# Kernel tuning notes

Measured on AMD Instinct MI355X. Metric: run time of the kernel, lower is better.

The kernel has to match this reference:

```python
import jax, jax.numpy as jnp
import numpy as np

N = 50000        # nodes
E = 800000       # edges (before self-loops)
IN = 128         # in_channels
HID = 32         # hidden_channels
HEADS = 8        # num_heads
G = 64           # num graphs in batch
NEG_SLOPE = 0.2  # PyG GATConv default


def setup_inputs() -> dict:
    key = jax.random.key(0)
    ks = jax.random.split(key, 12)
    x = jax.random.normal(ks[0], (N, IN), jnp.float32)
    edge_index = jax.random.randint(ks[1], (2, E), 0, N, jnp.int32)
    edge_attr = jax.random.normal(ks[2], (E, 4), jnp.float32)
    batch = jnp.sort(jax.random.randint(ks[3], (N,), 0, G, jnp.int32))
    s = 0.05
    # GATConv 1: in -> HEADS*HID
    W1 = jax.random.normal(ks[4], (IN, HEADS * HID), jnp.float32) * s
    a_src1 = jax.random.normal(ks[5], (HEADS, HID), jnp.float32) * s
    a_dst1 = jax.random.normal(ks[6], (HEADS, HID), jnp.float32) * s
    b1 = jnp.zeros((HEADS * HID,), jnp.float32)
    # GATConv 2: HEADS*HID -> HID (heads=1)
    W2 = jax.random.normal(ks[7], (HEADS * HID, HID), jnp.float32) * s
    a_src2 = jax.random.normal(ks[8], (1, HID), jnp.float32) * s
    a_dst2 = jax.random.normal(ks[9], (1, HID), jnp.float32) * s
    b2 = jnp.zeros((HID,), jnp.float32)
    return {"x": x, "edge_index": edge_index, "edge_attr": edge_attr, "batch": batch,
            "W1": W1, "a_src1": a_src1, "a_dst1": a_dst1, "b1": b1,
            "W2": W2, "a_src2": a_src2, "a_dst2": a_dst2, "b2": b2}


def gat_conv(x, src, dst, W, a_src, a_dst, b):
    # x: [N, F_in]; W: [F_in, H*C]; a_src/a_dst: [H, C]
    H, C = a_src.shape
    h = (x @ W).reshape(N, H, C)                      # [N, H, C]
    al_s = jnp.einsum('nhc,hc->nh', h, a_src)         # [N, H]
    al_d = jnp.einsum('nhc,hc->nh', h, a_dst)
    e = jax.nn.leaky_relu(al_s[src] + al_d[dst], NEG_SLOPE)  # [Etot, H]
    # segment softmax over incoming edges of each dst node
    m = jax.ops.segment_max(e, dst, num_segments=N)
    p = jnp.exp(e - m[dst])
    z = jax.ops.segment_sum(p, dst, num_segments=N)
    alpha = p / z[dst]                                # [Etot, H]
    out = jax.ops.segment_sum(alpha[:, :, None] * h[src], dst, num_segments=N)
    return out.reshape(N, H * C) + b


def reference(x, edge_index, edge_attr, batch, W1, a_src1, a_dst1, b1, W2, a_src2, a_dst2, b2):
    # edge_attr is ignored: GATConv was built without edge_dim (PyG lin_edge=None).
    loops = jnp.arange(N, dtype=edge_index.dtype)     # PyG add_self_loops=True
    src = jnp.concatenate([edge_index[0], loops])
    dst = jnp.concatenate([edge_index[1], loops])
    h = jax.nn.relu(gat_conv(x, src, dst, W1, a_src1, a_dst1, b1))
    # dropout p=0.2 is identity in eval mode
    h = gat_conv(h, src, dst, W2, a_src2, a_dst2, b2)  # [N, HID]
    # global_mean_pool over graph ids
    sums = jax.ops.segment_sum(h, batch, num_segments=G)
    cnts = jax.ops.segment_sum(jnp.ones((N, 1), h.dtype), batch, num_segments=G)
    return sums / jnp.maximum(cnts, 1.0)              # [G, HID]
```

## Files before the change

### kernel.cpp

```cpp
#include <hip/hip_runtime.h>
#include <hip/hip_bf16.h>

#define NNODES 50000
#define NEDGES 800000
#define FIN 128
#define HID 32
#define HEADS 8
#define NG 64
#define NEG_SLOPE 0.2f
#define MAXDEG 64

using bf16x8 = __attribute__((ext_vector_type(8))) short;
using f32x4  = __attribute__((ext_vector_type(4))) float;
using f32x2  = __attribute__((ext_vector_type(2))) float;

static __device__ __forceinline__ float leaky(float x) {
    return x > 0.f ? x : NEG_SLOPE * x;
}
static __device__ __forceinline__ unsigned short f2bf(float f) {
    unsigned int x = __float_as_uint(f);
    return (unsigned short)((x + 0x7FFFu + ((x >> 16) & 1u)) >> 16);
}
static __device__ __forceinline__ unsigned int pack2bf(float lo, float hi) {
    return (unsigned int)f2bf(lo) | ((unsigned int)f2bf(hi) << 16);
}
static __device__ __forceinline__ float bfl(unsigned int u) {
    return __uint_as_float(u << 16);
}
static __device__ __forceinline__ float bfh(unsigned int u) {
    return __uint_as_float(u & 0xFFFF0000u);
}
static __device__ __forceinline__ float bfs(unsigned short u) {
    return __uint_as_float((unsigned int)u << 16);
}
static __device__ __forceinline__ unsigned char f2fp8(float f) {
    return (unsigned char)(__builtin_amdgcn_cvt_pk_fp8_f32(f, f, 0, false) & 0xFF);
}

#define ZERO_BLOCKS 196
__global__ void zero_swz_kernel(int* __restrict__ cnt,
                                const float* __restrict__ W1, const float* __restrict__ W2,
                                const float* __restrict__ a_src1, const float* __restrict__ a_dst1,
                                unsigned short* __restrict__ w1s,
                                unsigned short* __restrict__ w2s,
                                unsigned short* __restrict__ w1al) {
    if (blockIdx.x < ZERO_BLOCKS) {
        int i = blockIdx.x * 256 + threadIdx.x;
        if (i < NNODES) cnt[i] = 0;
        return;
    }
    int idx = (blockIdx.x - ZERO_BLOCKS) * 256 + threadIdx.x;
    if (idx < 32768) {
        int j    = idx & 7;
        int lane = (idx >> 3) & 63;
        int ks   = (idx >> 9) & 3;
        int ct   = idx >> 11;
        int k = ks * 32 + (lane >> 4) * 8 + j;
        int n = ct * 16 + (lane & 15);
        w1s[idx] = f2bf(W1[k * 256 + n]);
    } else if (idx < 32768 + 8192) {
        int id2  = idx - 32768;
        int j    = id2 & 7;
        int lane = (id2 >> 3) & 63;
        int ks   = (id2 >> 9) & 7;
        int ct   = id2 >> 12;
        int k = ks * 32 + (lane >> 4) * 8 + j;
        int n = ct * 16 + (lane & 15);
        w2s[id2] = f2bf(W2[k * 32 + n]);
    } else if (idx < 32768 + 8192 + 2048) {
        int id3  = idx - 40960;
        int j    = id3 & 7;
        int lane = (id3 >> 3) & 63;
        int ks   = id3 >> 9;
        int k = ks * 32 + (lane >> 4) * 8 + j;
        int c = lane & 15;
        int h = c & 7;
        const float* av = (c < 8) ? a_src1 : a_dst1;
        float v = 0.f;
#pragma unroll 8
        for (int cc = 0; cc < 32; ++cc)
            v += W1[k * 256 + h * 32 + cc] * av[h * 32 + cc];
        w1al[id3] = f2bf(v);
    }
}

#define SCAT_GROUPS 782
__global__ void scatter_kernel(const int* __restrict__ ei, int* __restrict__ cnt,
                               unsigned short* __restrict__ csr) {
    int xcd = blockIdx.x & 7;
    int slice = blockIdx.x >> 3;
    int e4 = slice * 256 + threadIdx.x;
    int dlo = xcd * 6250;
    int dhi = dlo + 6250;
    if (e4 < NEDGES / 4) {
        int4 d = *(const int4*)(ei + NEDGES + e4 * 4);
        int4 s;
        bool a0 = d.x >= dlo && d.x < dhi;
        bool a1 = d.y >= dlo && d.y < dhi;
        bool a2 = d.z >= dlo && d.z < dhi;
        bool a3 = d.w >= dlo && d.w < dhi;
        if (a0 | a1 | a2 | a3) s = *(const int4*)(ei + e4 * 4);
        if (a0) { int p = atomicAdd(&cnt[d.x], 1); csr[(d.x << 6) + p] = (unsigned short)s.x; }
        if (a1) { int p = atomicAdd(&cnt[d.y], 1); csr[(d.y << 6) + p] = (unsigned short)s.y; }
        if (a2) { int p = atomicAdd(&cnt[d.z], 1); csr[(d.z << 6) + p] = (unsigned short)s.z; }
        if (a3) { int p = atomicAdd(&cnt[d.w], 1); csr[(d.w << 6) + p] = (unsigned short)s.w; }
    }
}

__global__ __launch_bounds__(256) void gemm1_mfma_kernel(const float* __restrict__ x,
                                                         const unsigned short* __restrict__ w1s,
                                                         const unsigned short* __restrict__ w1al,
                                                         unsigned char* __restrict__ h1f8,
                                                         float* __restrict__ al_s,
                                                         float* __restrict__ al_d) {
    int t = threadIdx.x;
    int w = t >> 6;
    int l = t & 63;
    int lane16 = l & 15, quad = l >> 4;

    bf16x8 bf[4][4];
    const bf16x8* wp = (const bf16x8*)w1s;
#pragma unroll
    for (int ct = 0; ct < 4; ++ct)
#pragma unroll
        for (int ks = 0; ks < 4; ++ks)
            bf[ct][ks] = wp[((w * 4 + ct) * 4 + ks) * 64 + l];

    bf16x8 bf_al[4];
    if (w == 0) {
        const bf16x8* ap = (const bf16x8*)w1al;
#pragma unroll
        for (int ks = 0; ks < 4; ++ks)
            bf_al[ks] = ap[ks * 64 + l];
    }

    int rbase = blockIdx.x * 64;
    for (int rg = 0; rg < 4; ++rg) {
        int row0 = rbase + rg * 16;
        int r = row0 + lane16;
        int r_eff = r < NNODES ? r : NNODES - 1;
        bf16x8 af[4];
#pragma unroll
        for (int ks = 0; ks < 4; ++ks) {
            const float* ap = x + (size_t)r_eff * FIN + ks * 32 + quad * 8;
            float4 a0 = *(const float4*)ap;
            float4 a1 = *(const float4*)(ap + 4);
            bf16x8 v;
            v[0] = (short)f2bf(a0.x); v[1] = (short)f2bf(a0.y);
            v[2] = (short)f2bf(a0.z); v[3] = (short)f2bf(a0.w);
            v[4] = (short)f2bf(a1.x); v[5] = (short)f2bf(a1.y);
            v[6] = (short)f2bf(a1.z); v[7] = (short)f2bf(a1.w);
            af[ks] = v;
        }
        f32x4 acc[4];
#pragma unroll
        for (int ct = 0; ct < 4; ++ct) acc[ct] = (f32x4){0.f, 0.f, 0.f, 0.f};
#pragma unroll
        for (int ks = 0; ks < 4; ++ks)
#pragma unroll
            for (int ct = 0; ct < 4; ++ct)
                acc[ct] = __builtin_amdgcn_mfma_f32_16x16x32_bf16(af[ks], bf[ct][ks], acc[ct], 0, 0, 0);

        if (w == 0) {
            f32x4 aal = (f32x4){0.f, 0.f, 0.f, 0.f};
#pragma unroll
            for (int ks = 0; ks < 4; ++ks)
                aal = __builtin_amdgcn_mfma_f32_16x16x32_bf16(af[ks], bf_al[ks], aal, 0, 0, 0);
#pragma unroll
            for (int reg = 0; reg < 4; ++reg) {
                int gr = row0 + quad * 4 + reg;
                if (gr < NNODES) {
                    if (lane16 < 8) al_s[gr * HEADS + lane16] = aal[reg];
                    else            al_d[gr * HEADS + lane16 - 8] = aal[reg];
                }
            }
        }

#pragma unroll
        for (int ct = 0; ct < 4; ++ct)
#pragma unroll
            for (int reg = 0; reg < 4; ++reg) {
                int gr = row0 + quad * 4 + reg;
                if (gr < NNODES)
                    h1f8[(size_t)gr * 256 + w * 64 + ct * 16 + lane16] = f2fp8(acc[ct][reg]);
            }
    }
}

__global__ __launch_bounds__(256) void gather1_kernel(const unsigned char* __restrict__ h1f8,
                                                      const float* __restrict__ al_s,
                                                      const float* __restrict__ al_d,
                                                      const int* __restrict__ cnt,
                                                      const unsigned short* __restrict__ csr,
                                                      const float* __restrict__ b1,
                                                      unsigned short* __restrict__ out1b) {
    int t = threadIdx.x;
    int l = t & 63;
    int q = l & 31;
    int base = l & 32;
    int n = blockIdx.x * 8 + (t >> 5);
    int e_st = q >> 3;
    int h_st = q & 7;
    int h_f  = q >> 2;
    float ad_st = al_d[n * HEADS + h_st];

    float p = __expf(leaky(al_s[n * HEADS + h_f] + al_d[n * HEADS + h_f]));
    float z = p;
    f32x2 acc01, acc23, acc45, acc67;
    {
        uint2 v = *(const uint2*)(h1f8 + (size_t)n * 256 + q * 8);
        f32x2 pp = (f32x2){p, p};
        acc01 = pp * __builtin_amdgcn_cvt_pk_f32_fp8(v.x, false);
        acc23 = pp * __builtin_amdgcn_cvt_pk_f32_fp8(v.x, true);
        acc45 = pp * __builtin_amdgcn_cvt_pk_f32_fp8(v.y, false);
        acc67 = pp * __builtin_amdgcn_cvt_pk_f32_fp8(v.y, true);
    }

    int beg = n << 6;
    int end = beg + cnt[n];
    for (int i = beg; i < end; i += 4) {
        int rem = end - i;
        int src4 = n;
        float pe4 = 0.f;
        if (e_st < rem) {
            src4 = csr[i + e_st];
            pe4 = __expf(leaky(al_s[src4 * HEADS + h_st] + ad_st));
        }
#pragma unroll
        for (int j = 0; j < 4; ++j) {
            int   sj  = __shfl(src4, base + j * 8);
            float pej = __shfl(pe4, base + j * 8 + h_f);
            uint2 v = *(const uint2*)(h1f8 + (size_t)sj * 256 + q * 8);
            z += pej;
            f32x2 pj = (f32x2){pej, pej};
            acc01 += pj * __builtin_amdgcn_cvt_pk_f32_fp8(v.x, false);
            acc23 += pj * __builtin_amdgcn_cvt_pk_f32_fp8(v.x, true);
            acc45 += pj * __builtin_amdgcn_cvt_pk_f32_fp8(v.y, false);
            acc67 += pj * __builtin_amdgcn_cvt_pk_f32_fp8(v.y, true);
        }
    }
    float inv = 1.0f / z;
    float4 b0 = *(const float4*)(b1 + q * 8);
    float4 b2 = *(const float4*)(b1 + q * 8 + 4);
    float o[8];
    o[0] = acc01[0] * inv + b0.x; o[1] = acc01[1] * inv + b0.y;
    o[2] = acc23[0] * inv + b0.z; o[3] = acc23[1] * inv + b0.w;
    o[4] = acc45[0] * inv + b2.x; o[5] = acc45[1] * inv + b2.y;
    o[6] = acc67[0] * inv + b2.z; o[7] = acc67[1] * inv + b2.w;
#pragma unroll
    for (int k = 0; k < 8; ++k) o[k] = o[k] > 0.f ? o[k] : 0.f;
    uint4 pk;
    pk.x = pack2bf(o[0], o[1]); pk.y = pack2bf(o[2], o[3]);
    pk.z = pack2bf(o[4], o[5]); pk.w = pack2bf(o[6], o[7]);
    *(uint4*)(out1b + (size_t)n * 256 + q * 8) = pk;
}

__global__ __launch_bounds__(256) void gemm2_mfma_kernel(const unsigned short* __restrict__ out1b,
                                                         const unsigned short* __restrict__ w2s,
                                                         const float* __restrict__ a_src,
                                                         const float* __restrict__ a_dst,
                                                         unsigned short* __restrict__ h2b,
                                                         float* __restrict__ al_s,
                                                         float* __restrict__ al_d) {
    int t = threadIdx.x;
    int w = t >> 6;
    int l = t & 63;
    int lane16 = l & 15, quad = l >> 4;

    bf16x8 bf[2][8];
    const bf16x8* wp = (const bf16x8*)w2s;
#pragma unroll
    for (int ct = 0; ct < 2; ++ct)
#pragma unroll
        for (int ks = 0; ks < 8; ++ks)
            bf[ct][ks] = wp[((ct * 8 + ks)) * 64 + l];

    float as_c[2], ad_c[2];
#pragma unroll
    for (int ct = 0; ct < 2; ++ct) {
        as_c[ct] = a_src[ct * 16 + lane16];
        ad_c[ct] = a_dst[ct * 16 + lane16];
    }

    int row0 = blockIdx.x * 64 + w * 16;
    int r = row0 + lane16;
    int r_eff = r < NNODES ? r : NNODES - 1;
    f32x4 acc[2];
    acc[0] = (f32x4){0.f, 0.f, 0.f, 0.f};
    acc[1] = (f32x4){0.f, 0.f, 0.f, 0.f};
#pragma unroll
    for (int ks = 0; ks < 8; ++ks) {
        bf16x8 af = *(const bf16x8*)(out1b + (size_t)r_eff * 256 + ks * 32 + quad * 8);
        acc[0] = __builtin_amdgcn_mfma_f32_16x16x32_bf16(af, bf[0][ks], acc[0], 0, 0, 0);
        acc[1] = __builtin_amdgcn_mfma_f32_16x16x32_bf16(af, bf[1][ks], acc[1], 0, 0, 0);
    }
#pragma unroll
    for (int reg = 0; reg < 4; ++reg) {
        int gr = row0 + quad * 4 + reg;
        if (gr < NNODES) {
            h2b[(size_t)gr * 32 + lane16]      = f2bf(acc[0][reg]);
            h2b[(size_t)gr * 32 + 16 + lane16] = f2bf(acc[1][reg]);
        }
        float ps = acc[0][reg] * as_c[0] + acc[1][reg] * as_c[1];
        float pd = acc[0][reg] * ad_c[0] + acc[1][reg] * ad_c[1];
#pragma unroll
        for (int m = 1; m < 16; m <<= 1) {
            ps += __shfl_xor(ps, m);
            pd += __shfl_xor(pd, m);
        }
        if (lane16 == 0 && gr < NNODES) {
            al_s[gr] = ps;
            al_d[gr] = pd;
        }
    }
}

__global__ __launch_bounds__(256) void gather2_kernel(const unsigned short* __restrict__ h2b,
                                                      const float* __restrict__ al_s,
                                                      const float* __restrict__ al_d,
                                                      const int* __restrict__ cnt,
                                                      const unsigned short* __restrict__ csr,
                                                      const float* __restrict__ b2,
                                                      float* __restrict__ out2) {
    int t = threadIdx.x;
    int l = t & 63;
    int e_sl = l & 15;
    int base = l & 48;
    int c0 = (l & 15) * 2;
    int n = blockIdx.x * 16 + (t >> 4);

    float ad = al_d[n];
    float p = __expf(leaky(al_s[n] + ad));
    float z = p;
    float acc0, acc1;
    {
        unsigned int v = *(const unsigned int*)(h2b + (size_t)n * HID + c0);
        acc0 = p * bfl(v);
        acc1 = p * bfh(v);
    }
    int beg = n << 6;
    int end = beg + cnt[n];
    for (int i = beg; i < end; i += 16) {
        int rem = end - i;
        int src = n;
        float pe = 0.f;
        if (e_sl < rem) {
            src = csr[i + e_sl];
            pe = __expf(leaky(al_s[src] + ad));
        }
        int m = rem < 16 ? rem : 16;
        for (int j0 = 0; j0 < m; j0 += 8) {
#pragma unroll
            for (int jj = 0; jj < 8; ++jj) {
                int   sj  = __shfl(src, base + j0 + jj);
                float pej = __shfl(pe, base + j0 + jj);
                unsigned int v = *(const unsigned int*)(h2b + (size_t)sj * HID + c0);
                z += pej;
                acc0 += pej * bfl(v);
                acc1 += pej * bfh(v);
            }
        }
    }
    float inv = 1.0f / z;
    float2 o;
    o.x = acc0 * inv + b2[c0];
    o.y = acc1 * inv + b2[c0 + 1];
    *(float2*)(out2 + (size_t)n * HID + c0) = o;
}

__global__ __launch_bounds__(256) void pool_kernel(const float* __restrict__ out2,
                                                   const int* __restrict__ batch,
                                                   float* __restrict__ out) {
    __shared__ float red[256];
    int g = blockIdx.x;
    int t = threadIdx.x;
    int c = t & 31;
    int sub = t >> 5;
    int beg, end;
    {
        int lo = 0, hi = NNODES;
        while (lo < hi) { int mid = (lo + hi) >> 1; if (batch[mid] < g) lo = mid + 1; else hi = mid; }
        beg = lo;
        lo = beg; hi = NNODES;
        while (lo < hi) { int mid = (lo + hi) >> 1; if (batch[mid] < g + 1) lo = mid + 1; else hi = mid; }
        end = lo;
    }
    float s = 0.f;
    for (int n = beg + sub; n < end; n += 8) s += out2[n * HID + c];
    red[t] = s;
    __syncthreads();
    if (t < 32) {
        float tot = 0.f;
#pragma unroll
        for (int k = 0; k < 8; ++k) tot += red[c + 32 * k];
        int cnt2 = end - beg;
        out[g * HID + c] = tot / (float)(cnt2 > 0 ? cnt2 : 1);
    }
}

extern "C" void kernel_launch(void* const* d_in, const int* in_sizes, int n_in,
                              void* d_out, int out_size, void* d_ws, size_t ws_size,
                              hipStream_t stream) {
    const float* x      = (const float*)d_in[0];
    const int*   ei     = (const int*)d_in[1];
    const int*   batch  = (const int*)d_in[3];
    const float* W1     = (const float*)d_in[4];
    const float* a_src1 = (const float*)d_in[5];
    const float* a_dst1 = (const float*)d_in[6];
    const float* b1     = (const float*)d_in[7];
    const float* W2     = (const float*)d_in[8];
    const float* a_src2 = (const float*)d_in[9];
    const float* a_dst2 = (const float*)d_in[10];
    const float* b2     = (const float*)d_in[11];
    float* out = (float*)d_out;

    char* ws = (char*)d_ws;
    size_t off = 0;
    auto alloc = [&](size_t bytes) {
        size_t o = off;
        off = (off + bytes + 255) & ~(size_t)255;
        return o;
    };
    unsigned char*  h1f8  = (unsigned char*)(ws + alloc((size_t)NNODES * 256));
    unsigned short* out1b = (unsigned short*)(ws + alloc((size_t)NNODES * 256 * 2));
    unsigned short* h2b   = (unsigned short*)(ws + alloc((size_t)NNODES * HID * 2));
    unsigned short* w1s   = (unsigned short*)(ws + alloc((size_t)16 * 4 * 64 * 8 * 2));
    unsigned short* w2s   = (unsigned short*)(ws + alloc((size_t)2 * 8 * 64 * 8 * 2));
    unsigned short* w1al  = (unsigned short*)(ws + alloc((size_t)4 * 64 * 8 * 2));
    float* out2   = (float*)(ws + alloc((size_t)NNODES * HID * 4));
    float* al_s1  = (float*)(ws + alloc((size_t)NNODES * HEADS * 4));
    float* al_d1  = (float*)(ws + alloc((size_t)NNODES * HEADS * 4));
    float* al_s2  = (float*)(ws + alloc((size_t)NNODES * 4));
    float* al_d2  = (float*)(ws + alloc((size_t)NNODES * 4));
    int*   cnt    = (int*)(ws + alloc((size_t)NNODES * 4));
    unsigned short* csr = (unsigned short*)(ws + alloc((size_t)NNODES * MAXDEG * 2));
    (void)ws_size;

    zero_swz_kernel<<<ZERO_BLOCKS + 168, 256, 0, stream>>>(cnt, W1, W2, a_src1, a_dst1,
                                                           w1s, w2s, w1al);
    scatter_kernel<<<SCAT_GROUPS * 8, 256, 0, stream>>>(ei, cnt, csr);

    gemm1_mfma_kernel<<<(NNODES + 63) / 64, 256, 0, stream>>>(x, w1s, w1al,
                                                              h1f8, al_s1, al_d1);
    gather1_kernel<<<NNODES / 8, 256, 0, stream>>>(h1f8, al_s1, al_d1, cnt, csr, b1, out1b);

    gemm2_mfma_kernel<<<(NNODES + 63) / 64, 256, 0, stream>>>(out1b, w2s, a_src2, a_dst2,
                                                              h2b, al_s2, al_d2);
    gather2_kernel<<<NNODES / 16, 256, 0, stream>>>(h2b, al_s2, al_d2, cnt, csr, b2, out2);
    pool_kernel<<<NG, 256, 0, stream>>>(out2, batch, out);
}
```

Before: 253.6 us.

## Partition layer-1 features by head pair and pin partitions to XCDs

Layer-1 fp8 features are stored head-pair-major (four 64-byte planes per node), and the attention logits are stored head-major. Each gather block handles one head pair for 32 nodes, and the block index is mapped so that every XCD reads only one 3.2 MB feature plane, which should keep that plane resident in its L2. The change also uses nontemporal loads for CSR indices and nontemporal stores for the output. In exchange, each node's CSR list and exp computations are now repeated across four head-pair blocks, and each edge gather reads a 64-byte segment instead of a full 256-byte row.

```diff
diff --git a/kernel.cpp b/kernel.cpp
--- a/kernel.cpp
+++ b/kernel.cpp
@@ -13,6 +13,7 @@
 using bf16x8 = __attribute__((ext_vector_type(8))) short;
 using f32x4  = __attribute__((ext_vector_type(4))) float;
 using f32x2  = __attribute__((ext_vector_type(2))) float;
+using u32x4  = __attribute__((ext_vector_type(4))) unsigned int;
 
 static __device__ __forceinline__ float leaky(float x) {
     return x > 0.f ? x : NEG_SLOPE * x;
@@ -110,7 +111,7 @@
 __global__ __launch_bounds__(256) void gemm1_mfma_kernel(const float* __restrict__ x,
                                                          const unsigned short* __restrict__ w1s,
                                                          const unsigned short* __restrict__ w1al,
-                                                         unsigned char* __restrict__ h1f8,
+                                                         unsigned char* __restrict__ h1p,
                                                          float* __restrict__ al_s,
                                                          float* __restrict__ al_d) {
     int t = threadIdx.x;
@@ -170,8 +171,8 @@
             for (int reg = 0; reg < 4; ++reg) {
                 int gr = row0 + quad * 4 + reg;
                 if (gr < NNODES) {
-                    if (lane16 < 8) al_s[gr * HEADS + lane16] = aal[reg];
-                    else            al_d[gr * HEADS + lane16 - 8] = aal[reg];
+                    if (lane16 < 8) al_s[(size_t)lane16 * NNODES + gr] = aal[reg];
+                    else            al_d[(size_t)(lane16 - 8) * NNODES + gr] = aal[reg];
                 }
             }
         }
@@ -182,33 +183,41 @@
             for (int reg = 0; reg < 4; ++reg) {
                 int gr = row0 + quad * 4 + reg;
                 if (gr < NNODES)
-                    h1f8[(size_t)gr * 256 + w * 64 + ct * 16 + lane16] = f2fp8(acc[ct][reg]);
+                    h1p[((size_t)w * NNODES + gr) * 64 + ct * 16 + lane16] = f2fp8(acc[ct][reg]);
             }
     }
 }
 
-__global__ __launch_bounds__(256) void gather1_kernel(const unsigned char* __restrict__ h1f8,
+__global__ __launch_bounds__(256) void gather1_kernel(const unsigned char* __restrict__ h1p,
                                                       const float* __restrict__ al_s,
                                                       const float* __restrict__ al_d,
                                                       const int* __restrict__ cnt,
                                                       const unsigned short* __restrict__ csr,
                                                       const float* __restrict__ b1,
                                                       unsigned short* __restrict__ out1b) {
+    int b = blockIdx.x;
+    int xcd = b & 7;
+    int hp = xcd >> 1;
+    int g = (b >> 3) * 2 + (xcd & 1);
     int t = threadIdx.x;
     int l = t & 63;
-    int q = l & 31;
-    int base = l & 32;
-    int n = blockIdx.x * 8 + (t >> 5);
-    int e_st = q >> 3;
-    int h_st = q & 7;
-    int h_f  = q >> 2;
-    float ad_st = al_d[n * HEADS + h_st];
-
-    float p = __expf(leaky(al_s[n * HEADS + h_f] + al_d[n * HEADS + h_f]));
+    int base = l & 56;
+    int rr = l & 7;
+    int hs = rr >> 2;
+    int e_slot = rr & 3;
+    int n = g * 32 + (t >> 3);
+    if (n >= NNODES) return;
+
+    int h = hp * 2 + hs;
+    const float* als_h = al_s + (size_t)h * NNODES;
+    float ad = al_d[(size_t)h * NNODES + n];
+    const unsigned char* hrow = h1p + (size_t)hp * NNODES * 64;
+
+    float p = __expf(leaky(als_h[n] + ad));
     float z = p;
     f32x2 acc01, acc23, acc45, acc67;
     {
-        uint2 v = *(const uint2*)(h1f8 + (size_t)n * 256 + q * 8);
+        uint2 v = *(const uint2*)(hrow + (size_t)n * 64 + rr * 8);
         f32x2 pp = (f32x2){p, p};
         acc01 = pp * __builtin_amdgcn_cvt_pk_f32_fp8(v.x, false);
         acc23 = pp * __builtin_amdgcn_cvt_pk_f32_fp8(v.x, true);
@@ -222,15 +231,16 @@
         int rem = end - i;
         int src4 = n;
         float pe4 = 0.f;
-        if (e_st < rem) {
-            src4 = csr[i + e_st];
-            pe4 = __expf(leaky(al_s[src4 * HEADS + h_st] + ad_st));
+        if (e_slot < rem) {
+            src4 = __builtin_nontemporal_load(&csr[i + e_slot]);
+            pe4 = __expf(leaky(als_h[src4] + ad));
         }
 #pragma unroll
         for (int j = 0; j < 4; ++j) {
-            int   sj  = __shfl(src4, base + j * 8);
-            float pej = __shfl(pe4, base + j * 8 + h_f);
-            uint2 v = *(const uint2*)(h1f8 + (size_t)sj * 256 + q * 8);
+            int idx = base + hs * 4 + j;
+            int   sj  = __shfl(src4, idx);
+            float pej = __shfl(pe4, idx);
+            uint2 v = *(const uint2*)(hrow + (size_t)sj * 64 + rr * 8);
             z += pej;
             f32x2 pj = (f32x2){pej, pej};
             acc01 += pj * __builtin_amdgcn_cvt_pk_f32_fp8(v.x, false);
@@ -240,8 +250,8 @@
         }
     }
     float inv = 1.0f / z;
-    float4 b0 = *(const float4*)(b1 + q * 8);
-    float4 b2 = *(const float4*)(b1 + q * 8 + 4);
+    float4 b0 = *(const float4*)(b1 + hp * 64 + rr * 8);
+    float4 b2 = *(const float4*)(b1 + hp * 64 + rr * 8 + 4);
     float o[8];
     o[0] = acc01[0] * inv + b0.x; o[1] = acc01[1] * inv + b0.y;
     o[2] = acc23[0] * inv + b0.z; o[3] = acc23[1] * inv + b0.w;
@@ -249,10 +259,10 @@
     o[6] = acc67[0] * inv + b2.z; o[7] = acc67[1] * inv + b2.w;
 #pragma unroll
     for (int k = 0; k < 8; ++k) o[k] = o[k] > 0.f ? o[k] : 0.f;
-    uint4 pk;
-    pk.x = pack2bf(o[0], o[1]); pk.y = pack2bf(o[2], o[3]);
-    pk.z = pack2bf(o[4], o[5]); pk.w = pack2bf(o[6], o[7]);
-    *(uint4*)(out1b + (size_t)n * 256 + q * 8) = pk;
+    u32x4 pk;
+    pk[0] = pack2bf(o[0], o[1]); pk[1] = pack2bf(o[2], o[3]);
+    pk[2] = pack2bf(o[4], o[5]); pk[3] = pack2bf(o[6], o[7]);
+    __builtin_nontemporal_store(pk, (u32x4*)(out1b + (size_t)n * 256 + hp * 64 + rr * 8));
 }
 
 __global__ __launch_bounds__(256) void gemm2_mfma_kernel(const unsigned short* __restrict__ out1b,
@@ -421,7 +431,7 @@
         off = (off + bytes + 255) & ~(size_t)255;
         return o;
     };
-    unsigned char*  h1f8  = (unsigned char*)(ws + alloc((size_t)NNODES * 256));
+    unsigned char*  h1p   = (unsigned char*)(ws + alloc((size_t)NNODES * 256));
     unsigned short* out1b = (unsigned short*)(ws + alloc((size_t)NNODES * 256 * 2));
     unsigned short* h2b   = (unsigned short*)(ws + alloc((size_t)NNODES * HID * 2));
     unsigned short* w1s   = (unsigned short*)(ws + alloc((size_t)16 * 4 * 64 * 8 * 2));
@@ -441,8 +451,8 @@
     scatter_kernel<<<SCAT_GROUPS * 8, 256, 0, stream>>>(ei, cnt, csr);
 
     gemm1_mfma_kernel<<<(NNODES + 63) / 64, 256, 0, stream>>>(x, w1s, w1al,
-                                                              h1f8, al_s1, al_d1);
-    gather1_kernel<<<NNODES / 8, 256, 0, stream>>>(h1f8, al_s1, al_d1, cnt, csr, b1, out1b);
+                                                              h1p, al_s1, al_d1);
+    gather1_kernel<<<8 * 782, 256, 0, stream>>>(h1p, al_s1, al_d1, cnt, csr, b1, out1b);
 
     gemm2_mfma_kernel<<<(NNODES + 63) / 64, 256, 0, stream>>>(out1b, w2s, a_src2, a_dst2,
                                                               h2b, al_s2, al_d2);
```

After: 296.4 us. +16.9%, slower.

## Map gather blocks to XCD-local node ranges and prefetch next edge chunk

Applied to the files above, without the earlier changes.

Both gather kernels now assign destination nodes so that each XCD (blockIdx & 7) handles a contiguous range of nodes. This matches the ranges the scatter kernel used when writing cnt/csr, so those entries should already sit in that XCD's L2. The edge loops are also software-pipelined: the next chunk's source indices and attention exponentials are loaded and computed before the current chunk is accumulated, to hide csr/al_s latency. The grids are padded slightly and extra threads exit early. The pipelining adds some register pressure.

```diff
diff --git a/kernel.cpp b/kernel.cpp
--- a/kernel.cpp
+++ b/kernel.cpp
@@ -9,6 +9,7 @@
 #define NG 64
 #define NEG_SLOPE 0.2f
 #define MAXDEG 64
+#define NPX 6250
 
 using bf16x8 = __attribute__((ext_vector_type(8))) short;
 using f32x4  = __attribute__((ext_vector_type(4))) float;
@@ -29,9 +30,6 @@
 }
 static __device__ __forceinline__ float bfh(unsigned int u) {
     return __uint_as_float(u & 0xFFFF0000u);
-}
-static __device__ __forceinline__ float bfs(unsigned short u) {
-    return __uint_as_float((unsigned int)u << 16);
 }
 static __device__ __forceinline__ unsigned char f2fp8(float f) {
     return (unsigned char)(__builtin_amdgcn_cvt_pk_fp8_f32(f, f, 0, false) & 0xFF);
@@ -90,8 +88,8 @@
     int xcd = blockIdx.x & 7;
     int slice = blockIdx.x >> 3;
     int e4 = slice * 256 + threadIdx.x;
-    int dlo = xcd * 6250;
-    int dhi = dlo + 6250;
+    int dlo = xcd * NPX;
+    int dhi = dlo + NPX;
     if (e4 < NEDGES / 4) {
         int4 d = *(const int4*)(ei + NEDGES + e4 * 4);
         int4 s;
@@ -187,6 +185,7 @@
     }
 }
 
+#define G1_SLICES 782
 __global__ __launch_bounds__(256) void gather1_kernel(const unsigned char* __restrict__ h1f8,
                                                       const float* __restrict__ al_s,
                                                       const float* __restrict__ al_d,
@@ -194,11 +193,16 @@
                                                       const unsigned short* __restrict__ csr,
                                                       const float* __restrict__ b1,
                                                       unsigned short* __restrict__ out1b) {
+    int b = blockIdx.x;
+    int xcd = b & 7;
+    int slice = b >> 3;
     int t = threadIdx.x;
     int l = t & 63;
     int q = l & 31;
     int base = l & 32;
-    int n = blockIdx.x * 8 + (t >> 5);
+    int ln = slice * 8 + (t >> 5);
+    if (ln >= NPX) return;
+    int n = xcd * NPX + ln;
     int e_st = q >> 3;
     int h_st = q & 7;
     int h_f  = q >> 2;
@@ -217,19 +221,26 @@
     }
 
     int beg = n << 6;
-    int end = beg + cnt[n];
+    int dg  = cnt[n];
+    int end = beg + dg;
+    int   src_c = n;
+    float pe_c  = 0.f;
+    if (e_st < dg) {
+        src_c = csr[beg + e_st];
+        pe_c = __expf(leaky(al_s[src_c * HEADS + h_st] + ad_st));
+    }
     for (int i = beg; i < end; i += 4) {
-        int rem = end - i;
-        int src4 = n;
-        float pe4 = 0.f;
-        if (e_st < rem) {
-            src4 = csr[i + e_st];
-            pe4 = __expf(leaky(al_s[src4 * HEADS + h_st] + ad_st));
+        int remn = end - (i + 4);
+        int   src_n = n;
+        float pe_n  = 0.f;
+        if (e_st < remn) {
+            src_n = csr[i + 4 + e_st];
+            pe_n = __expf(leaky(al_s[src_n * HEADS + h_st] + ad_st));
         }
 #pragma unroll
         for (int j = 0; j < 4; ++j) {
-            int   sj  = __shfl(src4, base + j * 8);
-            float pej = __shfl(pe4, base + j * 8 + h_f);
+            int   sj  = __shfl(src_c, base + j * 8);
+            float pej = __shfl(pe_c, base + j * 8 + h_f);
             uint2 v = *(const uint2*)(h1f8 + (size_t)sj * 256 + q * 8);
             z += pej;
             f32x2 pj = (f32x2){pej, pej};
@@ -238,6 +249,7 @@
             acc45 += pj * __builtin_amdgcn_cvt_pk_f32_fp8(v.y, false);
             acc67 += pj * __builtin_amdgcn_cvt_pk_f32_fp8(v.y, true);
         }
+        src_c = src_n; pe_c = pe_n;
     }
     float inv = 1.0f / z;
     float4 b0 = *(const float4*)(b1 + q * 8);
@@ -315,6 +327,7 @@
     }
 }
 
+#define G2_SLICES 391
 __global__ __launch_bounds__(256) void gather2_kernel(const unsigned short* __restrict__ h2b,
                                                       const float* __restrict__ al_s,
                                                       const float* __restrict__ al_d,
@@ -322,12 +335,17 @@
                                                       const unsigned short* __restrict__ csr,
                                                       const float* __restrict__ b2,
                                                       float* __restrict__ out2) {
+    int b = blockIdx.x;
+    int xcd = b & 7;
+    int slice = b >> 3;
     int t = threadIdx.x;
     int l = t & 63;
     int e_sl = l & 15;
     int base = l & 48;
     int c0 = (l & 15) * 2;
-    int n = blockIdx.x * 16 + (t >> 4);
+    int ln = slice * 16 + (t >> 4);
+    if (ln >= NPX) return;
+    int n = xcd * NPX + ln;
 
     float ad = al_d[n];
     float p = __expf(leaky(al_s[n] + ad));
@@ -339,27 +357,35 @@
         acc1 = p * bfh(v);
     }
     int beg = n << 6;
-    int end = beg + cnt[n];
+    int dg  = cnt[n];
+    int end = beg + dg;
+    int   src_c = n;
+    float pe_c  = 0.f;
+    if (e_sl < dg) {
+        src_c = csr[beg + e_sl];
+        pe_c = __expf(leaky(al_s[src_c] + ad));
+    }
     for (int i = beg; i < end; i += 16) {
-        int rem = end - i;
-        int src = n;
-        float pe = 0.f;
-        if (e_sl < rem) {
-            src = csr[i + e_sl];
-            pe = __expf(leaky(al_s[src] + ad));
-        }
-        int m = rem < 16 ? rem : 16;
+        int remn = end - (i + 16);
+        int   src_n = n;
+        float pe_n  = 0.f;
+        if (e_sl < remn) {
+            src_n = csr[i + 16 + e_sl];
+            pe_n = __expf(leaky(al_s[src_n] + ad));
+        }
+        int m = end - i < 16 ? end - i : 16;
         for (int j0 = 0; j0 < m; j0 += 8) {
 #pragma unroll
             for (int jj = 0; jj < 8; ++jj) {
-                int   sj  = __shfl(src, base + j0 + jj);
-                float pej = __shfl(pe, base + j0 + jj);
+                int   sj  = __shfl(src_c, base + j0 + jj);
+                float pej = __shfl(pe_c, base + j0 + jj);
                 unsigned int v = *(const unsigned int*)(h2b + (size_t)sj * HID + c0);
                 z += pej;
                 acc0 += pej * bfl(v);
                 acc1 += pej * bfh(v);
             }
         }
+        src_c = src_n; pe_c = pe_n;
     }
     float inv = 1.0f / z;
     float2 o;
@@ -442,10 +468,10 @@
 
     gemm1_mfma_kernel<<<(NNODES + 63) / 64, 256, 0, stream>>>(x, w1s, w1al,
                                                               h1f8, al_s1, al_d1);
-    gather1_kernel<<<NNODES / 8, 256, 0, stream>>>(h1f8, al_s1, al_d1, cnt, csr, b1, out1b);
+    gather1_kernel<<<8 * G1_SLICES, 256, 0, stream>>>(h1f8, al_s1, al_d1, cnt, csr, b1, out1b);
 
     gemm2_mfma_kernel<<<(NNODES + 63) / 64, 256, 0, stream>>>(out1b, w2s, a_src2, a_dst2,
                                                               h2b, al_s2, al_d2);
-    gather2_kernel<<<NNODES / 16, 256, 0, stream>>>(h2b, al_s2, al_d2, cnt, csr, b2, out2);
+    gather2_kernel<<<8 * G2_SLICES, 256, 0, stream>>>(h2b, al_s2, al_d2, cnt, csr, b2, out2);
     pool_kernel<<<NG, 256, 0, stream>>>(out2, batch, out);
 }
```

New measurement: 252.9 us. About the same (-0.3%).
